# Optimization experiments

Measured on AMD Instinct MI355X. Metric: run time of the kernel, lower is better.

Reference implementation:

```python
import jax, jax.numpy as jnp
from jax import lax
import numpy as np

B, N, CIN, COUT, HID = 16, 4096, 64, 128, 128
RATIO, K = 0.25, 32
M = int(N * RATIO)  # 1024 sampled centroids per cloud


def setup_inputs() -> dict:
    key = jax.random.key(0)
    ks = jax.random.split(key, 6)
    s = 0.02
    return {
        "x": jax.random.normal(ks[0], (B, N, CIN), jnp.float32),
        "pos": jax.random.normal(ks[1], (B, N, 3), jnp.float32),
        "W1": jax.random.normal(ks[2], (CIN + 3, HID), jnp.float32) * s,
        "b1": jnp.zeros((HID,), jnp.float32),
        "W2": jax.random.normal(ks[3], (HID, COUT), jnp.float32) * s,
        "b2": jnp.zeros((COUT,), jnp.float32),
        "Wlin": jax.random.normal(ks[4], (CIN, COUT), jnp.float32) * s,
        "blin": jnp.zeros((COUT,), jnp.float32),
    }


def mish(v):
    return v * jnp.tanh(jax.nn.softplus(v))


def fps(pc, m):
    # Farthest point sampling (deterministic start at index 0, as PyG with random_start=False).
    n = pc.shape[0]

    def step(carry, _):
        mind, last = carry
        d = jnp.sum((pc - pc[last]) ** 2, axis=-1)  # [N]
        mind = jnp.minimum(mind, d)
        nxt = jnp.argmax(mind).astype(jnp.int32)
        return (mind, nxt), nxt

    init = (jnp.full((n,), np.inf, pc.dtype), jnp.int32(0))
    _, rest = lax.scan(step, init, None, length=m - 1)
    return jnp.concatenate([jnp.zeros((1,), jnp.int32), rest])  # [M]


def reference(x, pos, W1, b1, W2, b2, Wlin, blin):
    def per_cloud(xc, pc):
        # xc: [N,CIN], pc: [N,3]
        idx = fps(pc, M)                                        # [M]
        q = pc[idx]                                             # [M,3] sampled centroids
        d2 = jnp.sum((q[:, None, :] - pc[None, :, :]) ** 2, -1)  # [M,N]
        _, nbr = lax.top_k(-d2, K)                              # [M,K] knn indices
        rel = pc[nbr] - q[:, None, :]                           # [M,K,3]
        h = jnp.concatenate([xc[nbr], rel], axis=-1)            # [M,K,CIN+3]
        h = mish(h @ W1 + b1)                                   # local_nn layer 1
        h = h @ W2 + b2                                         # [M,K,COUT]
        agg = jnp.max(h, axis=1)                                # PointNetConv max aggregation
        out = agg + xc[idx] @ Wlin + blin                       # residual skip via self.lin
        return out, q

    x_out, pos_out = jax.vmap(per_cloud)(x, pos)
    return x_out, pos_out
```

## Files before the change

kernel.cpp:

```cpp
#include <hip/hip_runtime.h>
#include <hip/hip_bf16.h>

constexpr int B    = 16;
constexpr int N    = 4096;
constexpr int CIN  = 64;
constexpr int COUT = 128;
constexpr int M    = 1024;
constexpr int K    = 32;

constexpr int K1  = 96;
constexpr int LDH = 136;
constexpr int NCONS = 240;
constexpr int PUBM  = 15;

typedef __attribute__((ext_vector_type(8))) short short8;
typedef __attribute__((ext_vector_type(4))) float f32x4;
typedef __attribute__((ext_vector_type(2))) float f32x2;

static __device__ __forceinline__ unsigned short f2bf(float f) {
  unsigned u = __float_as_uint(f);
  unsigned r = (u + 0x7FFFu + ((u >> 16) & 1u)) >> 16;
  return (unsigned short)r;
}

static __device__ __forceinline__ float fast_mish(float v) {
  float u = __expf(v);
  float s = u * (u + 2.0f);
  float t = s / (s + 2.0f);
  return (v > 60.f) ? v : v * t;
}

template <int CTRL, int RM>
static __device__ __forceinline__ unsigned dpp_umax_step(unsigned x) {
  int o = __builtin_amdgcn_update_dpp((int)x, (int)x, CTRL, RM, 0xF, false);
  unsigned u = (unsigned)o;
  return x > u ? x : u;
}
static __device__ __forceinline__ unsigned wave_umax(unsigned x) {
  x = dpp_umax_step<0x111, 0xF>(x);
  x = dpp_umax_step<0x112, 0xF>(x);
  x = dpp_umax_step<0x114, 0xF>(x);
  x = dpp_umax_step<0x118, 0xF>(x);
  x = dpp_umax_step<0x142, 0xA>(x);
  x = dpp_umax_step<0x143, 0xC>(x);
  return (unsigned)__builtin_amdgcn_readlane((int)x, 63);
}

static __device__ __forceinline__ unsigned long long umax64(unsigned long long a,
                                                            unsigned long long b) {
  return a > b ? a : b;
}

__global__ __launch_bounds__(256) void prep_weights(const float* __restrict__ W1,
                                                    const float* __restrict__ W2,
                                                    unsigned short* __restrict__ W1t,
                                                    unsigned short* __restrict__ W2t) {
  const int n = blockIdx.x;
  const int t = threadIdx.x;
  if (t < K1) {
    W1t[n * K1 + t] = (t < 67) ? f2bf(W1[t * 128 + n]) : (unsigned short)0;
  } else if (t < K1 + 128) {
    int k = t - K1;
    W2t[n * 128 + k] = f2bf(W2[k * 128 + n]);
  }
}

__global__ __launch_bounds__(512) void mega_kernel(
    const float* __restrict__ x, const float* __restrict__ pos,
    const unsigned short* __restrict__ W1t, const unsigned short* __restrict__ W2t,
    const float* __restrict__ b1, const float* __restrict__ b2,
    const float* __restrict__ Wlin, const float* __restrict__ blin,
    int* __restrict__ idx, int* __restrict__ progress, float* __restrict__ pos4,
    float* __restrict__ xout, float* __restrict__ pout) {
  __shared__ __align__(16) unsigned char smem[86016];
  const int tid = threadIdx.x;

  if (blockIdx.x < B) {
#pragma clang fp contract(off)
    const int b = blockIdx.x;
    float(*sp)[4] = (float(*)[4])smem;
    unsigned long long(*skey)[8] = (unsigned long long(*)[8])(smem + 65536);
    const float* p = pos + (size_t)b * (N * 3);
    float* p4 = pos4 + (size_t)b * N * 4;

    f32x2 px2[4], py2[4], pz2[4];
    float mind[8];
#pragma unroll
    for (int j = 0; j < 8; j++) {
      const int n = tid + j * 512;
      const float xx = p[3 * n + 0];
      const float yy = p[3 * n + 1];
      const float zz = p[3 * n + 2];
      px2[j >> 1][j & 1] = xx;
      py2[j >> 1][j & 1] = yy;
      pz2[j >> 1][j & 1] = zz;
      mind[j] = __builtin_inff();
      f32x4 v;
      v[0] = xx; v[1] = yy; v[2] = zz; v[3] = 0.f;
      *(f32x4*)(&sp[n][0]) = v;
      *(f32x4*)(p4 + 4 * n) = v;
    }
    float qx = p[0], qy = p[1], qz = p[2];
    if (tid == 0) {
      idx[b * M + 0] = 0;
      pout[(size_t)(b * M + 0) * 3 + 0] = qx;
      pout[(size_t)(b * M + 0) * 3 + 1] = qy;
      pout[(size_t)(b * M + 0) * 3 + 2] = qz;
    }
    __syncthreads();

    const int wv = tid >> 6, lane = tid & 63;
    for (int t = 1; t < M; t++) {
      const f32x2 nqx = {-qx, -qx};
      const f32x2 nqy = {-qy, -qy};
      const f32x2 nqz = {-qz, -qz};
      float bv = -1.f;
      unsigned bn = 0;
#pragma unroll
      for (int k = 0; k < 4; k++) {
        f32x2 dx = px2[k] + nqx;
        f32x2 dy = py2[k] + nqy;
        f32x2 dz = pz2[k] + nqz;
        f32x2 s = (dx * dx + dy * dy) + dz * dz;
        const float mi0 = fminf(mind[2 * k + 0], s.x);
        mind[2 * k + 0] = mi0;
        bool c0 = mi0 > bv;
        bv = c0 ? mi0 : bv;
        bn = c0 ? (unsigned)(tid + (2 * k + 0) * 512) : bn;
        const float mi1 = fminf(mind[2 * k + 1], s.y);
        mind[2 * k + 1] = mi1;
        bool c1 = mi1 > bv;
        bv = c1 ? mi1 : bv;
        bn = c1 ? (unsigned)(tid + (2 * k + 1) * 512) : bn;
      }
      const unsigned vb = __float_as_uint(bv);
      const unsigned wb = wave_umax(vb);
      unsigned tk = (vb == wb) ? ~bn : 0u;
      tk = wave_umax(tk);
      const int par = t & 1;
      if (lane == 0) skey[par][wv] = ((unsigned long long)wb << 32) | tk;
      __syncthreads();
      const unsigned long long k0 = skey[par][0];
      const unsigned long long k1 = skey[par][1];
      const unsigned long long k2 = skey[par][2];
      const unsigned long long k3 = skey[par][3];
      const unsigned long long k4 = skey[par][4];
      const unsigned long long k5 = skey[par][5];
      const unsigned long long k6 = skey[par][6];
      const unsigned long long k7 = skey[par][7];
      const unsigned long long bb =
          umax64(umax64(umax64(k0, k1), umax64(k2, k3)),
                 umax64(umax64(k4, k5), umax64(k6, k7)));
      const unsigned n = ~(unsigned)bb;
      const f32x4 qv = *(const f32x4*)(&sp[n][0]);
      qx = qv[0];
      qy = qv[1];
      qz = qv[2];
      if (tid == 0) {
        idx[b * M + t] = (int)n;
        pout[(size_t)(b * M + t) * 3 + 0] = qx;
        pout[(size_t)(b * M + t) * 3 + 1] = qy;
        pout[(size_t)(b * M + t) * 3 + 2] = qz;
        if ((t & PUBM) == PUBM) {
          __hip_atomic_store(progress + b, t + 1, __ATOMIC_RELEASE,
                             __HIP_MEMORY_SCOPE_AGENT);
        }
      }
    }
  } else {
    const int wv = tid >> 6, lane = tid & 63;
    const int lrow = lane & 15;
    const int g = lane >> 4;
    unsigned short* A2 = (unsigned short*)smem + wv * (32 * LDH);
    const int wgid = (blockIdx.x - B) * 8 + wv;

    for (int W = wgid; W < B * M; W += NCONS * 8) {
      const int b = W >> 10;
      const int t = W & (M - 1);
      int got = __hip_atomic_load(progress + b, __ATOMIC_ACQUIRE,
                                  __HIP_MEMORY_SCOPE_AGENT);
      while (got <= t) {
        __builtin_amdgcn_s_sleep(8);
        got = __hip_atomic_load(progress + b, __ATOMIC_ACQUIRE,
                                __HIP_MEMORY_SCOPE_AGENT);
      }
      const float* p4 = pos4 + (size_t)b * N * 4;
      const int sel = idx[W];
      const f32x4 q = *(const f32x4*)(p4 + 4 * sel);
      int n0 = 0, n1 = 0;
      {
#pragma clang fp contract(off)
        const f32x2 nqx = {-q[0], -q[0]};
        const f32x2 nqy = {-q[1], -q[1]};
        const f32x2 nqz = {-q[2], -q[2]};
        float d[64];
#pragma unroll
        for (int jj = 0; jj < 32; jj++) {
          const f32x4 v0 = *(const f32x4*)(p4 + 4 * ((2 * jj + 0) * 64 + lane));
          const f32x4 v1 = *(const f32x4*)(p4 + 4 * ((2 * jj + 1) * 64 + lane));
          f32x2 vx = {v0[0], v1[0]};
          f32x2 vy = {v0[1], v1[1]};
          f32x2 vz = {v0[2], v1[2]};
          f32x2 dx = vx + nqx;
          f32x2 dy = vy + nqy;
          f32x2 dz = vz + nqz;
          f32x2 s = (dx * dx + dy * dy) + dz * dz;
          d[2 * jj + 0] = s.x;
          d[2 * jj + 1] = s.y;
        }
        float gv[8];
        int gj[8];
#pragma unroll
        for (int gg = 0; gg < 8; gg++) {
          gv[gg] = __builtin_inff();
          gj[gg] = 8 * gg;
#pragma unroll
          for (int e = 0; e < 8; e++) {
            const int j = 8 * gg + e;
            bool c = d[j] < gv[gg];
            gv[gg] = c ? d[j] : gv[gg];
            gj[gg] = c ? j : gj[gg];
          }
        }
        for (int r = 0; r < K; r++) {
          float bv = __builtin_inff();
          int bj = 0;
#pragma unroll
          for (int gg = 0; gg < 8; gg++) {
            bool c = gv[gg] < bv;
            bv = c ? gv[gg] : bv;
            bj = c ? gj[gg] : bj;
          }
          const unsigned bn = (unsigned)(bj * 64 + lane);
          const unsigned nb = ~__float_as_uint(bv);
          const unsigned wnb = wave_umax(nb);
          unsigned tk = (nb == wnb) ? (0xFFFFFFFFu - bn) : 0u;
          tk = wave_umax(tk);
          const unsigned wn = 0xFFFFFFFFu - tk;
          n0 = (r == lrow) ? (int)wn : n0;
          n1 = (r == 16 + lrow) ? (int)wn : n1;
          const int wj = (int)(wn >> 6);
          const int wl = (int)(wn & 63);
          const int wg = wj >> 3;
#pragma unroll
          for (int gg = 0; gg < 8; gg++) {
            if (gg == wg) {
#pragma unroll
              for (int e = 0; e < 8; e++) {
                if (8 * gg + e == wj) {
                  if (lane == wl) d[8 * gg + e] = __builtin_inff();
                }
              }
              float nv = __builtin_inff();
              int nj = 8 * gg;
#pragma unroll
              for (int e = 0; e < 8; e++) {
                const int j = 8 * gg + e;
                bool c = d[j] < nv;
                nv = c ? d[j] : nv;
                nj = c ? j : nj;
              }
              gv[gg] = nv;
              gj[gg] = nj;
            }
          }
        }
      }

      const float qx = q[0], qy = q[1], qz = q[2];
      short8 a0[3], a1[3];
      {
        const float* xr0 = x + ((size_t)b * N + n0) * CIN;
        const float* xr1 = x + ((size_t)b * N + n1) * CIN;
#pragma unroll
        for (int kc = 0; kc < 2; kc++) {
          const int k0 = kc * 32 + g * 8;
          f32x4 u0 = *(const f32x4*)(xr0 + k0);
          f32x4 u1 = *(const f32x4*)(xr0 + k0 + 4);
          f32x4 v0 = *(const f32x4*)(xr1 + k0);
          f32x4 v1 = *(const f32x4*)(xr1 + k0 + 4);
          short8 ha, hb;
#pragma unroll
          for (int e = 0; e < 4; e++) {
            ha[e] = (short)f2bf(u0[e]);
            ha[e + 4] = (short)f2bf(u1[e]);
            hb[e] = (short)f2bf(v0[e]);
            hb[e + 4] = (short)f2bf(v1[e]);
          }
          a0[kc] = ha;
          a1[kc] = hb;
        }
        short8 z = {};
        a0[2] = z;
        a1[2] = z;
        if (g == 0) {
          float r0x = p4[4 * n0 + 0] - qx, r0y = p4[4 * n0 + 1] - qy, r0z = p4[4 * n0 + 2] - qz;
          float r1x = p4[4 * n1 + 0] - qx, r1y = p4[4 * n1 + 1] - qy, r1z = p4[4 * n1 + 2] - qz;
          a0[2][0] = (short)f2bf(r0x); a0[2][1] = (short)f2bf(r0y); a0[2][2] = (short)f2bf(r0z);
          a1[2][0] = (short)f2bf(r1x); a1[2][1] = (short)f2bf(r1y); a1[2][2] = (short)f2bf(r1z);
        }
      }

#pragma unroll 2
      for (int nt = 0; nt < 8; nt++) {
        const unsigned short* w1r = W1t + (size_t)(nt * 16 + lrow) * K1 + g * 8;
        f32x4 c0 = {}, c1 = {};
#pragma unroll
        for (int kc = 0; kc < 3; kc++) {
          short8 bfr = *(const short8*)(w1r + kc * 32);
          c0 = __builtin_amdgcn_mfma_f32_16x16x32_bf16(a0[kc], bfr, c0, 0, 0, 0);
          c1 = __builtin_amdgcn_mfma_f32_16x16x32_bf16(a1[kc], bfr, c1, 0, 0, 0);
        }
        const int colI = nt * 16 + lrow;
        const float bb = b1[colI];
#pragma unroll
        for (int reg = 0; reg < 4; reg++) {
          const int row = g * 4 + reg;
          A2[row * LDH + colI] = f2bf(fast_mish(c0[reg] + bb));
          A2[(16 + row) * LDH + colI] = f2bf(fast_mish(c1[reg] + bb));
        }
      }

      f32x4 xq[4];
      {
        const float* xs = x + ((size_t)b * N + sel) * CIN + g * 16;
#pragma unroll
        for (int v = 0; v < 4; v++) xq[v] = *(const f32x4*)(xs + 4 * v);
      }

#pragma unroll 2
      for (int nt = 0; nt < 8; nt++) {
        const unsigned short* w2r = W2t + (size_t)(nt * 16 + lrow) * 128 + g * 8;
        f32x4 c0 = {}, c1 = {};
#pragma unroll
        for (int kc = 0; kc < 4; kc++) {
          short8 af0 = *(const short8*)(A2 + lrow * LDH + kc * 32 + g * 8);
          short8 af1 = *(const short8*)(A2 + (16 + lrow) * LDH + kc * 32 + g * 8);
          short8 bfr = *(const short8*)(w2r + kc * 32);
          c0 = __builtin_amdgcn_mfma_f32_16x16x32_bf16(af0, bfr, c0, 0, 0, 0);
          c1 = __builtin_amdgcn_mfma_f32_16x16x32_bf16(af1, bfr, c1, 0, 0, 0);
        }
        float pm = fmaxf(fmaxf(fmaxf(c0[0], c0[1]), fmaxf(c0[2], c0[3])),
                         fmaxf(fmaxf(c1[0], c1[1]), fmaxf(c1[2], c1[3])));
        pm = fmaxf(pm, __shfl_xor(pm, 16, 64));
        pm = fmaxf(pm, __shfl_xor(pm, 32, 64));
        const int j = nt * 16 + lrow;
        float s = 0.f;
#pragma unroll
        for (int e = 0; e < 16; e++) {
          s += xq[e >> 2][e & 3] * Wlin[(g * 16 + e) * 128 + j];
        }
        s += __shfl_xor(s, 16, 64);
        s += __shfl_xor(s, 32, 64);
        if (g == 0) {
          xout[(size_t)W * 128 + j] = pm + b2[j] + s + blin[j];
        }
      }
    }
  }
}

extern "C" void kernel_launch(void* const* d_in, const int* in_sizes, int n_in,
                              void* d_out, int out_size, void* d_ws, size_t ws_size,
                              hipStream_t stream) {
  const float* x    = (const float*)d_in[0];
  const float* pos  = (const float*)d_in[1];
  const float* W1   = (const float*)d_in[2];
  const float* b1   = (const float*)d_in[3];
  const float* W2   = (const float*)d_in[4];
  const float* b2   = (const float*)d_in[5];
  const float* Wlin = (const float*)d_in[6];
  const float* blin = (const float*)d_in[7];

  float* out  = (float*)d_out;
  float* xout = out;
  float* pout = out + (size_t)B * M * COUT;

  char* ws = (char*)d_ws;
  int* idx            = (int*)ws;
  int* progress       = (int*)(ws + 65536);
  unsigned short* W1t = (unsigned short*)(ws + 65792);
  unsigned short* W2t = (unsigned short*)(ws + 90368);
  float* pos4         = (float*)(ws + 123136);

  prep_weights<<<dim3(128), dim3(256), 0, stream>>>(W1, W2, W1t, W2t);
  mega_kernel<<<dim3(B + NCONS), dim3(512), 0, stream>>>(
      x, pos, W1t, W2t, b1, b2, Wlin, blin, idx, progress, pos4, xout, pout);
}
```

Before: 1.057 ms.

## Relax producer-consumer sync: padded progress counters, relaxed atomics, longer spin sleep

Result: faster. 966.6 us (-8.6%).

```diff
diff --git a/kernel.cpp b/kernel.cpp
--- a/kernel.cpp
+++ b/kernel.cpp
@@ -12,6 +12,7 @@
 constexpr int LDH = 136;
 constexpr int NCONS = 240;
 constexpr int PUBM  = 15;
+constexpr int PSTRIDE = 32;
 
 typedef __attribute__((ext_vector_type(8))) short short8;
 typedef __attribute__((ext_vector_type(4))) float f32x4;
@@ -102,12 +103,16 @@
     }
     float qx = p[0], qy = p[1], qz = p[2];
     if (tid == 0) {
-      idx[b * M + 0] = 0;
-      pout[(size_t)(b * M + 0) * 3 + 0] = qx;
-      pout[(size_t)(b * M + 0) * 3 + 1] = qy;
-      pout[(size_t)(b * M + 0) * 3 + 2] = qz;
+      __hip_atomic_store(idx + b * M, 0, __ATOMIC_RELAXED, __HIP_MEMORY_SCOPE_AGENT);
+      __hip_atomic_store(pout + (size_t)(b * M) * 3 + 0, qx, __ATOMIC_RELAXED, __HIP_MEMORY_SCOPE_AGENT);
+      __hip_atomic_store(pout + (size_t)(b * M) * 3 + 1, qy, __ATOMIC_RELAXED, __HIP_MEMORY_SCOPE_AGENT);
+      __hip_atomic_store(pout + (size_t)(b * M) * 3 + 2, qz, __ATOMIC_RELAXED, __HIP_MEMORY_SCOPE_AGENT);
     }
     __syncthreads();
+    if (tid == 0) {
+      __hip_atomic_store(progress + b * PSTRIDE, 1, __ATOMIC_RELEASE,
+                         __HIP_MEMORY_SCOPE_AGENT);
+    }
 
     const int wv = tid >> 6, lane = tid & 63;
     for (int t = 1; t < M; t++) {
@@ -157,12 +162,13 @@
       qy = qv[1];
       qz = qv[2];
       if (tid == 0) {
-        idx[b * M + t] = (int)n;
-        pout[(size_t)(b * M + t) * 3 + 0] = qx;
-        pout[(size_t)(b * M + t) * 3 + 1] = qy;
-        pout[(size_t)(b * M + t) * 3 + 2] = qz;
+        __hip_atomic_store(idx + b * M + t, (int)n, __ATOMIC_RELAXED, __HIP_MEMORY_SCOPE_AGENT);
+        __hip_atomic_store(pout + (size_t)(b * M + t) * 3 + 0, qx, __ATOMIC_RELAXED, __HIP_MEMORY_SCOPE_AGENT);
+        __hip_atomic_store(pout + (size_t)(b * M + t) * 3 + 1, qy, __ATOMIC_RELAXED, __HIP_MEMORY_SCOPE_AGENT);
+        __hip_atomic_store(pout + (size_t)(b * M + t) * 3 + 2, qz, __ATOMIC_RELAXED, __HIP_MEMORY_SCOPE_AGENT);
         if ((t & PUBM) == PUBM) {
-          __hip_atomic_store(progress + b, t + 1, __ATOMIC_RELEASE,
+          asm volatile("s_waitcnt vmcnt(0)" ::: "memory");
+          __hip_atomic_store(progress + b * PSTRIDE, t + 1, __ATOMIC_RELAXED,
                              __HIP_MEMORY_SCOPE_AGENT);
         }
       }
@@ -177,15 +183,16 @@
     for (int W = wgid; W < B * M; W += NCONS * 8) {
       const int b = W >> 10;
       const int t = W & (M - 1);
-      int got = __hip_atomic_load(progress + b, __ATOMIC_ACQUIRE,
+      int got = __hip_atomic_load(progress + b * PSTRIDE, __ATOMIC_RELAXED,
                                   __HIP_MEMORY_SCOPE_AGENT);
       while (got <= t) {
-        __builtin_amdgcn_s_sleep(8);
-        got = __hip_atomic_load(progress + b, __ATOMIC_ACQUIRE,
+        __builtin_amdgcn_s_sleep(64);
+        got = __hip_atomic_load(progress + b * PSTRIDE, __ATOMIC_RELAXED,
                                 __HIP_MEMORY_SCOPE_AGENT);
       }
       const float* p4 = pos4 + (size_t)b * N * 4;
-      const int sel = idx[W];
+      const int sel = __hip_atomic_load(idx + W, __ATOMIC_RELAXED,
+                                        __HIP_MEMORY_SCOPE_AGENT);
       const f32x4 q = *(const f32x4*)(p4 + 4 * sel);
       int n0 = 0, n1 = 0;
       {
@@ -379,9 +386,9 @@
   char* ws = (char*)d_ws;
   int* idx            = (int*)ws;
   int* progress       = (int*)(ws + 65536);
-  unsigned short* W1t = (unsigned short*)(ws + 65792);
-  unsigned short* W2t = (unsigned short*)(ws + 90368);
-  float* pos4         = (float*)(ws + 123136);
+  unsigned short* W1t = (unsigned short*)(ws + 67584);
+  unsigned short* W2t = (unsigned short*)(ws + 92160);
+  float* pos4         = (float*)(ws + 124928);
 
   prep_weights<<<dim3(128), dim3(256), 0, stream>>>(W1, W2, W1t, W2t);
   mega_kernel<<<dim3(B + NCONS), dim3(512), 0, stream>>>(
```

## Split persistent producer-consumer megakernel into separate FPS and KNN-MLP kernels

Applied to the files above, without the earlier changes.

New measurement: 966.0 us. 8.6% less time.

```diff
diff --git a/kernel.cpp b/kernel.cpp
--- a/kernel.cpp
+++ b/kernel.cpp
@@ -10,8 +10,6 @@
 
 constexpr int K1  = 96;
 constexpr int LDH = 136;
-constexpr int NCONS = 240;
-constexpr int PUBM  = 15;
 
 typedef __attribute__((ext_vector_type(8))) short short8;
 typedef __attribute__((ext_vector_type(4))) float f32x4;
@@ -49,6 +47,100 @@
 static __device__ __forceinline__ unsigned long long umax64(unsigned long long a,
                                                             unsigned long long b) {
   return a > b ? a : b;
+}
+
+__global__ __launch_bounds__(512) void fps8_kernel(const float* __restrict__ pos,
+                                                   int* __restrict__ idx_out,
+                                                   float* __restrict__ pout,
+                                                   float* __restrict__ pos4) {
+#pragma clang fp contract(off)
+  const int b   = blockIdx.x;
+  const int tid = threadIdx.x;
+  __shared__ float sp[N][4];
+  __shared__ unsigned long long skey[2][8];
+  const float* p = pos + (size_t)b * (N * 3);
+  float* p4 = pos4 + (size_t)b * N * 4;
+
+  f32x2 px2[4], py2[4], pz2[4];
+  float mind[8];
+#pragma unroll
+  for (int j = 0; j < 8; j++) {
+    const int n = tid + j * 512;
+    const float x = p[3 * n + 0];
+    const float y = p[3 * n + 1];
+    const float z = p[3 * n + 2];
+    px2[j >> 1][j & 1] = x;
+    py2[j >> 1][j & 1] = y;
+    pz2[j >> 1][j & 1] = z;
+    mind[j] = __builtin_inff();
+    f32x4 v;
+    v[0] = x; v[1] = y; v[2] = z; v[3] = 0.f;
+    *(f32x4*)(&sp[n][0]) = v;
+    *(f32x4*)(p4 + 4 * n) = v;
+  }
+  float qx = p[0], qy = p[1], qz = p[2];
+  if (tid == 0) {
+    idx_out[b * M + 0] = 0;
+    pout[(size_t)(b * M + 0) * 3 + 0] = qx;
+    pout[(size_t)(b * M + 0) * 3 + 1] = qy;
+    pout[(size_t)(b * M + 0) * 3 + 2] = qz;
+  }
+  __syncthreads();
+
+  const int wv = tid >> 6, lane = tid & 63;
+  for (int t = 1; t < M; t++) {
+    const f32x2 nqx = {-qx, -qx};
+    const f32x2 nqy = {-qy, -qy};
+    const f32x2 nqz = {-qz, -qz};
+    float bv = -1.f;
+    unsigned bn = 0;
+#pragma unroll
+    for (int k = 0; k < 4; k++) {
+      f32x2 dx = px2[k] + nqx;
+      f32x2 dy = py2[k] + nqy;
+      f32x2 dz = pz2[k] + nqz;
+      f32x2 s = (dx * dx + dy * dy) + dz * dz;
+      const float mi0 = fminf(mind[2 * k + 0], s.x);
+      mind[2 * k + 0] = mi0;
+      bool c0 = mi0 > bv;
+      bv = c0 ? mi0 : bv;
+      bn = c0 ? (unsigned)(tid + (2 * k + 0) * 512) : bn;
+      const float mi1 = fminf(mind[2 * k + 1], s.y);
+      mind[2 * k + 1] = mi1;
+      bool c1 = mi1 > bv;
+      bv = c1 ? mi1 : bv;
+      bn = c1 ? (unsigned)(tid + (2 * k + 1) * 512) : bn;
+    }
+    const unsigned vb = __float_as_uint(bv);
+    const unsigned wb = wave_umax(vb);
+    unsigned tk = (vb == wb) ? ~bn : 0u;
+    tk = wave_umax(tk);
+    const int par = t & 1;
+    if (lane == 0) skey[par][wv] = ((unsigned long long)wb << 32) | tk;
+    __syncthreads();
+    const unsigned long long k0 = skey[par][0];
+    const unsigned long long k1 = skey[par][1];
+    const unsigned long long k2 = skey[par][2];
+    const unsigned long long k3 = skey[par][3];
+    const unsigned long long k4 = skey[par][4];
+    const unsigned long long k5 = skey[par][5];
+    const unsigned long long k6 = skey[par][6];
+    const unsigned long long k7 = skey[par][7];
+    const unsigned long long bb =
+        umax64(umax64(umax64(k0, k1), umax64(k2, k3)),
+               umax64(umax64(k4, k5), umax64(k6, k7)));
+    const unsigned n = ~(unsigned)bb;
+    const f32x4 qv = *(const f32x4*)(&sp[n][0]);
+    qx = qv[0];
+    qy = qv[1];
+    qz = qv[2];
+    if (tid == 0) {
+      idx_out[b * M + t] = (int)n;
+      pout[(size_t)(b * M + t) * 3 + 0] = qx;
+      pout[(size_t)(b * M + t) * 3 + 1] = qy;
+      pout[(size_t)(b * M + t) * 3 + 2] = qz;
+    }
+  }
 }
 
 __global__ __launch_bounds__(256) void prep_weights(const float* __restrict__ W1,
@@ -65,297 +157,192 @@
   }
 }
 
-__global__ __launch_bounds__(512) void mega_kernel(
-    const float* __restrict__ x, const float* __restrict__ pos,
+__global__ __launch_bounds__(256) void knnmlp_kernel(
+    const float* __restrict__ x, const float* __restrict__ pos4,
     const unsigned short* __restrict__ W1t, const unsigned short* __restrict__ W2t,
     const float* __restrict__ b1, const float* __restrict__ b2,
     const float* __restrict__ Wlin, const float* __restrict__ blin,
-    int* __restrict__ idx, int* __restrict__ progress, float* __restrict__ pos4,
-    float* __restrict__ xout, float* __restrict__ pout) {
-  __shared__ __align__(16) unsigned char smem[86016];
-  const int tid = threadIdx.x;
-
-  if (blockIdx.x < B) {
+    const int* __restrict__ idx, float* __restrict__ xout) {
+  __shared__ unsigned short sA2[4][32][LDH];
+  const int tid  = threadIdx.x;
+  const int wv   = tid >> 6;
+  const int lane = tid & 63;
+  const int lrow = lane & 15;
+  const int g    = lane >> 4;
+  unsigned short* A2 = &sA2[wv][0][0];
+  const int W = blockIdx.x * 4 + wv;
+  const int b = W >> 10;
+
+  const float* p4 = pos4 + (size_t)b * N * 4;
+  const int sel = idx[W];
+  const f32x4 q = *(const f32x4*)(p4 + 4 * sel);
+  int n0 = 0, n1 = 0;
+  {
 #pragma clang fp contract(off)
-    const int b = blockIdx.x;
-    float(*sp)[4] = (float(*)[4])smem;
-    unsigned long long(*skey)[8] = (unsigned long long(*)[8])(smem + 65536);
-    const float* p = pos + (size_t)b * (N * 3);
-    float* p4 = pos4 + (size_t)b * N * 4;
-
-    f32x2 px2[4], py2[4], pz2[4];
-    float mind[8];
-#pragma unroll
-    for (int j = 0; j < 8; j++) {
-      const int n = tid + j * 512;
-      const float xx = p[3 * n + 0];
-      const float yy = p[3 * n + 1];
-      const float zz = p[3 * n + 2];
-      px2[j >> 1][j & 1] = xx;
-      py2[j >> 1][j & 1] = yy;
-      pz2[j >> 1][j & 1] = zz;
-      mind[j] = __builtin_inff();
-      f32x4 v;
-      v[0] = xx; v[1] = yy; v[2] = zz; v[3] = 0.f;
-      *(f32x4*)(&sp[n][0]) = v;
-      *(f32x4*)(p4 + 4 * n) = v;
-    }
-    float qx = p[0], qy = p[1], qz = p[2];
-    if (tid == 0) {
-      idx[b * M + 0] = 0;
-      pout[(size_t)(b * M + 0) * 3 + 0] = qx;
-      pout[(size_t)(b * M + 0) * 3 + 1] = qy;
-      pout[(size_t)(b * M + 0) * 3 + 2] = qz;
-    }
-    __syncthreads();
-
-    const int wv = tid >> 6, lane = tid & 63;
-    for (int t = 1; t < M; t++) {
-      const f32x2 nqx = {-qx, -qx};
-      const f32x2 nqy = {-qy, -qy};
-      const f32x2 nqz = {-qz, -qz};
-      float bv = -1.f;
-      unsigned bn = 0;
-#pragma unroll
-      for (int k = 0; k < 4; k++) {
-        f32x2 dx = px2[k] + nqx;
-        f32x2 dy = py2[k] + nqy;
-        f32x2 dz = pz2[k] + nqz;
-        f32x2 s = (dx * dx + dy * dy) + dz * dz;
-        const float mi0 = fminf(mind[2 * k + 0], s.x);
-        mind[2 * k + 0] = mi0;
-        bool c0 = mi0 > bv;
-        bv = c0 ? mi0 : bv;
-        bn = c0 ? (unsigned)(tid + (2 * k + 0) * 512) : bn;
-        const float mi1 = fminf(mind[2 * k + 1], s.y);
-        mind[2 * k + 1] = mi1;
-        bool c1 = mi1 > bv;
-        bv = c1 ? mi1 : bv;
-        bn = c1 ? (unsigned)(tid + (2 * k + 1) * 512) : bn;
+    const f32x2 nqx = {-q[0], -q[0]};
+    const f32x2 nqy = {-q[1], -q[1]};
+    const f32x2 nqz = {-q[2], -q[2]};
+    float d[64];
+#pragma unroll
+    for (int jj = 0; jj < 32; jj++) {
+      const f32x4 v0 = *(const f32x4*)(p4 + 4 * ((2 * jj + 0) * 64 + lane));
+      const f32x4 v1 = *(const f32x4*)(p4 + 4 * ((2 * jj + 1) * 64 + lane));
+      f32x2 vx = {v0[0], v1[0]};
+      f32x2 vy = {v0[1], v1[1]};
+      f32x2 vz = {v0[2], v1[2]};
+      f32x2 dx = vx + nqx;
+      f32x2 dy = vy + nqy;
+      f32x2 dz = vz + nqz;
+      f32x2 s = (dx * dx + dy * dy) + dz * dz;
+      d[2 * jj + 0] = s.x;
+      d[2 * jj + 1] = s.y;
+    }
+    float gv[8];
+    int gj[8];
+#pragma unroll
+    for (int gg = 0; gg < 8; gg++) {
+      gv[gg] = __builtin_inff();
+      gj[gg] = 8 * gg;
+#pragma unroll
+      for (int e = 0; e < 8; e++) {
+        const int j = 8 * gg + e;
+        bool c = d[j] < gv[gg];
+        gv[gg] = c ? d[j] : gv[gg];
+        gj[gg] = c ? j : gj[gg];
       }
-      const unsigned vb = __float_as_uint(bv);
-      const unsigned wb = wave_umax(vb);
-      unsigned tk = (vb == wb) ? ~bn : 0u;
+    }
+    for (int r = 0; r < K; r++) {
+      float bv = __builtin_inff();
+      int bj = 0;
+#pragma unroll
+      for (int gg = 0; gg < 8; gg++) {
+        bool c = gv[gg] < bv;
+        bv = c ? gv[gg] : bv;
+        bj = c ? gj[gg] : bj;
+      }
+      const unsigned bn = (unsigned)(bj * 64 + lane);
+      const unsigned nb = ~__float_as_uint(bv);
+      const unsigned wnb = wave_umax(nb);
+      unsigned tk = (nb == wnb) ? (0xFFFFFFFFu - bn) : 0u;
       tk = wave_umax(tk);
-      const int par = t & 1;
-      if (lane == 0) skey[par][wv] = ((unsigned long long)wb << 32) | tk;
-      __syncthreads();
-      const unsigned long long k0 = skey[par][0];
-      const unsigned long long k1 = skey[par][1];
-      const unsigned long long k2 = skey[par][2];
-      const unsigned long long k3 = skey[par][3];
-      const unsigned long long k4 = skey[par][4];
-      const unsigned long long k5 = skey[par][5];
-      const unsigned long long k6 = skey[par][6];
-      const unsigned long long k7 = skey[par][7];
-      const unsigned long long bb =
-          umax64(umax64(umax64(k0, k1), umax64(k2, k3)),
-                 umax64(umax64(k4, k5), umax64(k6, k7)));
-      const unsigned n = ~(unsigned)bb;
-      const f32x4 qv = *(const f32x4*)(&sp[n][0]);
-      qx = qv[0];
-      qy = qv[1];
-      qz = qv[2];
-      if (tid == 0) {
-        idx[b * M + t] = (int)n;
-        pout[(size_t)(b * M + t) * 3 + 0] = qx;
-        pout[(size_t)(b * M + t) * 3 + 1] = qy;
-        pout[(size_t)(b * M + t) * 3 + 2] = qz;
-        if ((t & PUBM) == PUBM) {
-          __hip_atomic_store(progress + b, t + 1, __ATOMIC_RELEASE,
-                             __HIP_MEMORY_SCOPE_AGENT);
+      const unsigned wn = 0xFFFFFFFFu - tk;
+      n0 = (r == lrow) ? (int)wn : n0;
+      n1 = (r == 16 + lrow) ? (int)wn : n1;
+      const int wj = (int)(wn >> 6);
+      const int wl = (int)(wn & 63);
+      const int wg = wj >> 3;
+#pragma unroll
+      for (int gg = 0; gg < 8; gg++) {
+        if (gg == wg) {
+#pragma unroll
+          for (int e = 0; e < 8; e++) {
+            if (8 * gg + e == wj) {
+              if (lane == wl) d[8 * gg + e] = __builtin_inff();
+            }
+          }
+          float nv = __builtin_inff();
+          int nj = 8 * gg;
+#pragma unroll
+          for (int e = 0; e < 8; e++) {
+            const int j = 8 * gg + e;
+            bool c = d[j] < nv;
+            nv = c ? d[j] : nv;
+            nj = c ? j : nj;
+          }
+          gv[gg] = nv;
+          gj[gg] = nj;
         }
       }
     }
-  } else {
-    const int wv = tid >> 6, lane = tid & 63;
-    const int lrow = lane & 15;
-    const int g = lane >> 4;
-    unsigned short* A2 = (unsigned short*)smem + wv * (32 * LDH);
-    const int wgid = (blockIdx.x - B) * 8 + wv;
-
-    for (int W = wgid; W < B * M; W += NCONS * 8) {
-      const int b = W >> 10;
-      const int t = W & (M - 1);
-      int got = __hip_atomic_load(progress + b, __ATOMIC_ACQUIRE,
-                                  __HIP_MEMORY_SCOPE_AGENT);
-      while (got <= t) {
-        __builtin_amdgcn_s_sleep(8);
-        got = __hip_atomic_load(progress + b, __ATOMIC_ACQUIRE,
-                                __HIP_MEMORY_SCOPE_AGENT);
+  }
+
+  const float qx = q[0], qy = q[1], qz = q[2];
+  short8 a0[3], a1[3];
+  {
+    const float* xr0 = x + ((size_t)b * N + n0) * CIN;
+    const float* xr1 = x + ((size_t)b * N + n1) * CIN;
+#pragma unroll
+    for (int kc = 0; kc < 2; kc++) {
+      const int k0 = kc * 32 + g * 8;
+      f32x4 u0 = *(const f32x4*)(xr0 + k0);
+      f32x4 u1 = *(const f32x4*)(xr0 + k0 + 4);
+      f32x4 v0 = *(const f32x4*)(xr1 + k0);
+      f32x4 v1 = *(const f32x4*)(xr1 + k0 + 4);
+      short8 ha, hb;
+#pragma unroll
+      for (int e = 0; e < 4; e++) {
+        ha[e] = (short)f2bf(u0[e]);
+        ha[e + 4] = (short)f2bf(u1[e]);
+        hb[e] = (short)f2bf(v0[e]);
+        hb[e + 4] = (short)f2bf(v1[e]);
       }
-      const float* p4 = pos4 + (size_t)b * N * 4;
-      const int sel = idx[W];
-      const f32x4 q = *(const f32x4*)(p4 + 4 * sel);
-      int n0 = 0, n1 = 0;
-      {
-#pragma clang fp contract(off)
-        const f32x2 nqx = {-q[0], -q[0]};
-        const f32x2 nqy = {-q[1], -q[1]};
-        const f32x2 nqz = {-q[2], -q[2]};
-        float d[64];
-#pragma unroll
-        for (int jj = 0; jj < 32; jj++) {
-          const f32x4 v0 = *(const f32x4*)(p4 + 4 * ((2 * jj + 0) * 64 + lane));
-          const f32x4 v1 = *(const f32x4*)(p4 + 4 * ((2 * jj + 1) * 64 + lane));
-          f32x2 vx = {v0[0], v1[0]};
-          f32x2 vy = {v0[1], v1[1]};
-          f32x2 vz = {v0[2], v1[2]};
-          f32x2 dx = vx + nqx;
-          f32x2 dy = vy + nqy;
-          f32x2 dz = vz + nqz;
-          f32x2 s = (dx * dx + dy * dy) + dz * dz;
-          d[2 * jj + 0] = s.x;
-          d[2 * jj + 1] = s.y;
-        }
-        float gv[8];
-        int gj[8];
-#pragma unroll
-        for (int gg = 0; gg < 8; gg++) {
-          gv[gg] = __builtin_inff();
-          gj[gg] = 8 * gg;
-#pragma unroll
-          for (int e = 0; e < 8; e++) {
-            const int j = 8 * gg + e;
-            bool c = d[j] < gv[gg];
-            gv[gg] = c ? d[j] : gv[gg];
-            gj[gg] = c ? j : gj[gg];
-          }
-        }
-        for (int r = 0; r < K; r++) {
-          float bv = __builtin_inff();
-          int bj = 0;
-#pragma unroll
-          for (int gg = 0; gg < 8; gg++) {
-            bool c = gv[gg] < bv;
-            bv = c ? gv[gg] : bv;
-            bj = c ? gj[gg] : bj;
-          }
-          const unsigned bn = (unsigned)(bj * 64 + lane);
-          const unsigned nb = ~__float_as_uint(bv);
-          const unsigned wnb = wave_umax(nb);
-          unsigned tk = (nb == wnb) ? (0xFFFFFFFFu - bn) : 0u;
-          tk = wave_umax(tk);
-          const unsigned wn = 0xFFFFFFFFu - tk;
-          n0 = (r == lrow) ? (int)wn : n0;
-          n1 = (r == 16 + lrow) ? (int)wn : n1;
-          const int wj = (int)(wn >> 6);
-          const int wl = (int)(wn & 63);
-          const int wg = wj >> 3;
-#pragma unroll
-          for (int gg = 0; gg < 8; gg++) {
-            if (gg == wg) {
-#pragma unroll
-              for (int e = 0; e < 8; e++) {
-                if (8 * gg + e == wj) {
-                  if (lane == wl) d[8 * gg + e] = __builtin_inff();
-                }
-              }
-              float nv = __builtin_inff();
-              int nj = 8 * gg;
-#pragma unroll
-              for (int e = 0; e < 8; e++) {
-                const int j = 8 * gg + e;
-                bool c = d[j] < nv;
-                nv = c ? d[j] : nv;
-                nj = c ? j : nj;
-              }
-              gv[gg] = nv;
-              gj[gg] = nj;
-            }
-          }
-        }
-      }
-
-      const float qx = q[0], qy = q[1], qz = q[2];
-      short8 a0[3], a1[3];
-      {
-        const float* xr0 = x + ((size_t)b * N + n0) * CIN;
-        const float* xr1 = x + ((size_t)b * N + n1) * CIN;
-#pragma unroll
-        for (int kc = 0; kc < 2; kc++) {
-          const int k0 = kc * 32 + g * 8;
-          f32x4 u0 = *(const f32x4*)(xr0 + k0);
-          f32x4 u1 = *(const f32x4*)(xr0 + k0 + 4);
-          f32x4 v0 = *(const f32x4*)(xr1 + k0);
-          f32x4 v1 = *(const f32x4*)(xr1 + k0 + 4);
-          short8 ha, hb;
-#pragma unroll
-          for (int e = 0; e < 4; e++) {
-            ha[e] = (short)f2bf(u0[e]);
-            ha[e + 4] = (short)f2bf(u1[e]);
-            hb[e] = (short)f2bf(v0[e]);
-            hb[e + 4] = (short)f2bf(v1[e]);
-          }
-          a0[kc] = ha;
-          a1[kc] = hb;
-        }
-        short8 z = {};
-        a0[2] = z;
-        a1[2] = z;
-        if (g == 0) {
-          float r0x = p4[4 * n0 + 0] - qx, r0y = p4[4 * n0 + 1] - qy, r0z = p4[4 * n0 + 2] - qz;
-          float r1x = p4[4 * n1 + 0] - qx, r1y = p4[4 * n1 + 1] - qy, r1z = p4[4 * n1 + 2] - qz;
-          a0[2][0] = (short)f2bf(r0x); a0[2][1] = (short)f2bf(r0y); a0[2][2] = (short)f2bf(r0z);
-          a1[2][0] = (short)f2bf(r1x); a1[2][1] = (short)f2bf(r1y); a1[2][2] = (short)f2bf(r1z);
-        }
-      }
+      a0[kc] = ha;
+      a1[kc] = hb;
+    }
+    short8 z = {};
+    a0[2] = z;
+    a1[2] = z;
+    if (g == 0) {
+      float r0x = p4[4 * n0 + 0] - qx, r0y = p4[4 * n0 + 1] - qy, r0z = p4[4 * n0 + 2] - qz;
+      float r1x = p4[4 * n1 + 0] - qx, r1y = p4[4 * n1 + 1] - qy, r1z = p4[4 * n1 + 2] - qz;
+      a0[2][0] = (short)f2bf(r0x); a0[2][1] = (short)f2bf(r0y); a0[2][2] = (short)f2bf(r0z);
+      a1[2][0] = (short)f2bf(r1x); a1[2][1] = (short)f2bf(r1y); a1[2][2] = (short)f2bf(r1z);
+    }
+  }
 
 #pragma unroll 2
-      for (int nt = 0; nt < 8; nt++) {
-        const unsigned short* w1r = W1t + (size_t)(nt * 16 + lrow) * K1 + g * 8;
-        f32x4 c0 = {}, c1 = {};
-#pragma unroll
-        for (int kc = 0; kc < 3; kc++) {
-          short8 bfr = *(const short8*)(w1r + kc * 32);
-          c0 = __builtin_amdgcn_mfma_f32_16x16x32_bf16(a0[kc], bfr, c0, 0, 0, 0);
-          c1 = __builtin_amdgcn_mfma_f32_16x16x32_bf16(a1[kc], bfr, c1, 0, 0, 0);
-        }
-        const int colI = nt * 16 + lrow;
-        const float bb = b1[colI];
-#pragma unroll
-        for (int reg = 0; reg < 4; reg++) {
-          const int row = g * 4 + reg;
-          A2[row * LDH + colI] = f2bf(fast_mish(c0[reg] + bb));
-          A2[(16 + row) * LDH + colI] = f2bf(fast_mish(c1[reg] + bb));
-        }
-      }
-
-      f32x4 xq[4];
-      {
-        const float* xs = x + ((size_t)b * N + sel) * CIN + g * 16;
-#pragma unroll
-        for (int v = 0; v < 4; v++) xq[v] = *(const f32x4*)(xs + 4 * v);
-      }
+  for (int nt = 0; nt < 8; nt++) {
+    const unsigned short* w1r = W1t + (size_t)(nt * 16 + lrow) * K1 + g * 8;
+    f32x4 c0 = {}, c1 = {};
+#pragma unroll
+    for (int kc = 0; kc < 3; kc++) {
+      short8 bfr = *(const short8*)(w1r + kc * 32);
+      c0 = __builtin_amdgcn_mfma_f32_16x16x32_bf16(a0[kc], bfr, c0, 0, 0, 0);
+      c1 = __builtin_amdgcn_mfma_f32_16x16x32_bf16(a1[kc], bfr, c1, 0, 0, 0);
+    }
+    const int colI = nt * 16 + lrow;
+    const float bb = b1[colI];
+#pragma unroll
+    for (int reg = 0; reg < 4; reg++) {
+      const int row = g * 4 + reg;
+      A2[row * LDH + colI] = f2bf(fast_mish(c0[reg] + bb));
+      A2[(16 + row) * LDH + colI] = f2bf(fast_mish(c1[reg] + bb));
+    }
+  }
+
+  f32x4 xq[4];
+  {
+    const float* xs = x + ((size_t)b * N + sel) * CIN + g * 16;
+#pragma unroll
+    for (int v = 0; v < 4; v++) xq[v] = *(const f32x4*)(xs + 4 * v);
+  }
 
 #pragma unroll 2
-      for (int nt = 0; nt < 8; nt++) {
-        const unsigned short* w2r = W2t + (size_t)(nt * 16 + lrow) * 128 + g * 8;
-        f32x4 c0 = {}, c1 = {};
-#pragma unroll
-        for (int kc = 0; kc < 4; kc++) {
-          short8 af0 = *(const short8*)(A2 + lrow * LDH + kc * 32 + g * 8);
-          short8 af1 = *(const short8*)(A2 + (16 + lrow) * LDH + kc * 32 + g * 8);
-          short8 bfr = *(const short8*)(w2r + kc * 32);
-          c0 = __builtin_amdgcn_mfma_f32_16x16x32_bf16(af0, bfr, c0, 0, 0, 0);
-          c1 = __builtin_amdgcn_mfma_f32_16x16x32_bf16(af1, bfr, c1, 0, 0, 0);
-        }
-        float pm = fmaxf(fmaxf(fmaxf(c0[0], c0[1]), fmaxf(c0[2], c0[3])),
-                         fmaxf(fmaxf(c1[0], c1[1]), fmaxf(c1[2], c1[3])));
-        pm = fmaxf(pm, __shfl_xor(pm, 16, 64));
-        pm = fmaxf(pm, __shfl_xor(pm, 32, 64));
-        const int j = nt * 16 + lrow;
-        float s = 0.f;
-#pragma unroll
-        for (int e = 0; e < 16; e++) {
-          s += xq[e >> 2][e & 3] * Wlin[(g * 16 + e) * 128 + j];
-        }
-        s += __shfl_xor(s, 16, 64);
-        s += __shfl_xor(s, 32, 64);
-        if (g == 0) {
-          xout[(size_t)W * 128 + j] = pm + b2[j] + s + blin[j];
-        }
-      }
+  for (int nt = 0; nt < 8; nt++) {
+    const unsigned short* w2r = W2t + (size_t)(nt * 16 + lrow) * 128 + g * 8;
+    f32x4 c0 = {}, c1 = {};
+#pragma unroll
+    for (int kc = 0; kc < 4; kc++) {
+      short8 af0 = *(const short8*)(A2 + lrow * LDH + kc * 32 + g * 8);
+      short8 af1 = *(const short8*)(A2 + (16 + lrow) * LDH + kc * 32 + g * 8);
+      short8 bfr = *(const short8*)(w2r + kc * 32);
+      c0 = __builtin_amdgcn_mfma_f32_16x16x32_bf16(af0, bfr, c0, 0, 0, 0);
+      c1 = __builtin_amdgcn_mfma_f32_16x16x32_bf16(af1, bfr, c1, 0, 0, 0);
+    }
+    float pm = fmaxf(fmaxf(fmaxf(c0[0], c0[1]), fmaxf(c0[2], c0[3])),
+                     fmaxf(fmaxf(c1[0], c1[1]), fmaxf(c1[2], c1[3])));
+    pm = fmaxf(pm, __shfl_xor(pm, 16, 64));
+    pm = fmaxf(pm, __shfl_xor(pm, 32, 64));
+    const int j = nt * 16 + lrow;
+    float s = 0.f;
+#pragma unroll
+    for (int e = 0; e < 16; e++) {
+      s += xq[e >> 2][e & 3] * Wlin[(g * 16 + e) * 128 + j];
+    }
+    s += __shfl_xor(s, 16, 64);
+    s += __shfl_xor(s, 32, 64);
+    if (g == 0) {
+      xout[(size_t)W * 128 + j] = pm + b2[j] + s + blin[j];
     }
   }
 }
@@ -378,12 +365,12 @@
 
   char* ws = (char*)d_ws;
   int* idx            = (int*)ws;
-  int* progress       = (int*)(ws + 65536);
-  unsigned short* W1t = (unsigned short*)(ws + 65792);
-  unsigned short* W2t = (unsigned short*)(ws + 90368);
-  float* pos4         = (float*)(ws + 123136);
+  unsigned short* W1t = (unsigned short*)(ws + 65536);
+  unsigned short* W2t = (unsigned short*)(ws + 90112);
+  float* pos4         = (float*)(ws + 122880);
 
   prep_weights<<<dim3(128), dim3(256), 0, stream>>>(W1, W2, W1t, W2t);
-  mega_kernel<<<dim3(B + NCONS), dim3(512), 0, stream>>>(
-      x, pos, W1t, W2t, b1, b2, Wlin, blin, idx, progress, pos4, xout, pout);
-}
+  fps8_kernel<<<dim3(B), dim3(512), 0, stream>>>(pos, idx, pout, pos4);
+  knnmlp_kernel<<<dim3(B * M / 4), dim3(256), 0, stream>>>(
+      x, pos4, W1t, W2t, b1, b2, Wlin, blin, idx, xout);
+}
```
